# Performance work log

Hardware: AMD Instinct MI355X
Metric: run time of the kernel (lower is better)

The kernel has to match this reference:

```python
import jax, jax.numpy as jnp
import numpy as np

B, S, D, H = 2, 2048, 1024, 16
HD = D // H  # 64
ROPE_BASE = 10000.0


def setup_inputs() -> dict:
    key = jax.random.key(0)
    k1, k2, k3 = jax.random.split(key, 3)
    std = 1.0 / np.sqrt(D)
    x = jax.random.normal(k1, (B, S, D), dtype=jnp.float32)
    w_in = jax.random.normal(k2, (3 * D, D), dtype=jnp.float32) * std
    w_out = jax.random.normal(k3, (D, D), dtype=jnp.float32) * (std / np.sqrt(2.0))
    return {"x": x, "w_in": w_in, "w_out": w_out}


def _rope_cos_sin(seq_len, head_dim):
    inv_freq = 1.0 / (ROPE_BASE ** (jnp.arange(0, head_dim, 2, dtype=jnp.float32) / head_dim))
    t = jnp.arange(seq_len, dtype=jnp.float32)
    freqs = jnp.einsum("s,d->sd", t, inv_freq)          # [S, HD/2]
    emb = jnp.concatenate([freqs, freqs], axis=-1)       # [S, HD]
    return jnp.cos(emb)[None, :, None, :], jnp.sin(emb)[None, :, None, :]


def _rotate_half(x):
    x1, x2 = jnp.split(x, 2, axis=-1)
    return jnp.concatenate([-x2, x1], axis=-1)


def _apply_rope(x, cos, sin):
    return x * cos + _rotate_half(x) * sin


def reference(x, w_in, w_out):
    b, s, d = x.shape
    # fused QKV projection (no bias)
    qkv = x @ w_in.T                                      # [B, S, 3D]
    q, k, v = jnp.split(qkv, 3, axis=-1)
    q = q.reshape(b, s, H, HD)
    k = k.reshape(b, s, H, HD)
    v = v.reshape(b, s, H, HD)
    # rotary (offset = 0, no KV cache)
    cos, sin = _rope_cos_sin(s, HD)
    q = _apply_rope(q, cos, sin)
    k = _apply_rope(k, cos, sin)
    # causal SDPA, scale 1/sqrt(head_dim)
    scale = 1.0 / jnp.sqrt(jnp.asarray(HD, dtype=x.dtype))
    scores = jnp.einsum("bqhd,bkhd->bhqk", q, k) * scale  # [B, H, S, S]
    causal = jnp.tril(jnp.ones((s, s), dtype=bool))
    scores = jnp.where(causal, scores, jnp.asarray(-jnp.inf, dtype=scores.dtype))
    attn = jax.nn.softmax(scores, axis=-1)
    out = jnp.einsum("bhqk,bkhd->bqhd", attn, v).reshape(b, s, d)
    return out @ w_out.T
```

## Files before the change

kernel.cpp:

```cpp
#include <hip/hip_runtime.h>
#include <hip/hip_bf16.h>
#include <math.h>

#define NB 2
#define NS 2048
#define ND 1024
#define NH 16
#define HD 64
#define BS (NB*NS)
#define D3 (3*ND)
#define NT (NS/64)

typedef __bf16 bf16;
typedef __bf16 bf16x4 __attribute__((ext_vector_type(4)));
typedef __bf16 bf16x8 __attribute__((ext_vector_type(8)));
typedef float f32x4 __attribute__((ext_vector_type(4)));

#define MFMA16(a,b,c) __builtin_amdgcn_mfma_f32_16x16x32_bf16(a,b,c,0,0,0)

static __device__ inline f32x4 zero4() { f32x4 z; z[0]=0.f; z[1]=0.f; z[2]=0.f; z[3]=0.f; return z; }

__device__ __forceinline__ void gload_lds16(const bf16* g, bf16* l) {
    __builtin_amdgcn_global_load_lds(
        (__attribute__((address_space(1))) unsigned int*)g,
        (__attribute__((address_space(3))) unsigned int*)l, 16, 0, 0);
}

#define CVT1 (BS*ND/8)
#define CVT2 (D3*ND/8)
#define CVT3 (ND*ND/8)
#define CVTN (CVT1+CVT2+CVT3)
__global__ __launch_bounds__(256) void prep(
    const float* __restrict__ x, const float* __restrict__ w_in, const float* __restrict__ w_out,
    bf16* __restrict__ xb, bf16* __restrict__ winb, bf16* __restrict__ woutb,
    float* __restrict__ cosT, float* __restrict__ sinT)
{
    int i = blockIdx.x * 256 + threadIdx.x;
    if (i < CVTN) {
        const float* in; bf16* out; int j;
        if (i < CVT1)            { in = x;     out = xb;    j = i; }
        else if (i < CVT1+CVT2)  { in = w_in;  out = winb;  j = i - CVT1; }
        else                     { in = w_out; out = woutb; j = i - CVT1 - CVT2; }
        const float4* p = (const float4*)in;
        float4 a = p[j*2], b = p[j*2+1];
        bf16x8 o;
        o[0]=(bf16)a.x; o[1]=(bf16)a.y; o[2]=(bf16)a.z; o[3]=(bf16)a.w;
        o[4]=(bf16)b.x; o[5]=(bf16)b.y; o[6]=(bf16)b.z; o[7]=(bf16)b.w;
        ((bf16x8*)out)[j] = o;
    } else {
        int k = i - CVTN;
        int s = k >> 5, j = k & 31;
        float inv = __expf(-(float)j * (9.210340372f * 0.03125f));
        float ang = (float)s * inv;
        cosT[k] = cosf(ang);
        sinT[k] = sinf(ang);
    }
}

template<int EPI>
__global__ __launch_bounds__(256) void gemm_bt(
    const bf16* __restrict__ A, const bf16* __restrict__ Bm,
    float* __restrict__ C, bf16* __restrict__ Qb, bf16* __restrict__ Kb, bf16* __restrict__ Vt,
    const float* __restrict__ cosT, const float* __restrict__ sinT,
    int M, int N, int K)
{
    __shared__ bf16 As[2][128*64];
    __shared__ bf16 Bs[2][128*64];
    int t = threadIdx.x;
    int lane = t & 63, w = t >> 6;
    int wr = w >> 1, wc = w & 1;
    int lr = lane & 15, lg = lane >> 4;
    int m0 = blockIdx.y * 128, n0 = blockIdx.x * 128;

    int srow = lane >> 3;
    int schunk = (lane & 7) ^ srow;
    const bf16* gA = &A [(size_t)(m0 + w*32 + srow)*K + schunk*8];
    const bf16* gB = &Bm[(size_t)(n0 + w*32 + srow)*K + schunk*8];

    auto stage = [&](int kt) {
        int buf = kt & 1;
        bf16* lA = &As[buf][w*2048];
        bf16* lB = &Bs[buf][w*2048];
        int k0 = kt * 64;
        #pragma unroll
        for (int i=0;i<4;i++) {
            gload_lds16(gA + (size_t)(i*8)*K + k0, lA + i*512);
            gload_lds16(gB + (size_t)(i*8)*K + k0, lB + i*512);
        }
    };

    f32x4 acc[4][4];
    for (int m=0;m<4;m++) for (int n=0;n<4;n++) acc[m][n] = zero4();

    int nt = K >> 6;
    stage(0);
    stage(1);

    for (int kt = 0; kt < nt; kt++) {
        int cur = kt & 1;
        if (kt < nt-1) asm volatile("s_waitcnt vmcnt(8)" ::: "memory");
        else           asm volatile("s_waitcnt vmcnt(0)" ::: "memory");
        __builtin_amdgcn_s_barrier();
        __builtin_amdgcn_sched_barrier(0);

        bf16x8 af[2][4], bfr[2][4];
        #pragma unroll
        for (int ks=0;ks<2;ks++) {
            #pragma unroll
            for (int m=0;m<4;m++) {
                int row = wr*64 + m*16 + lr;
                af[ks][m] = *(const bf16x8*)&As[cur][row*64 + (((ks*4+lg) ^ (row&7))*8)];
            }
            #pragma unroll
            for (int n=0;n<4;n++) {
                int row = wc*64 + n*16 + lr;
                bfr[ks][n] = *(const bf16x8*)&Bs[cur][row*64 + (((ks*4+lg) ^ (row&7))*8)];
            }
        }
        asm volatile("s_waitcnt lgkmcnt(0)" ::: "memory");
        __builtin_amdgcn_sched_barrier(0);
        __builtin_amdgcn_s_barrier();
        __builtin_amdgcn_sched_barrier(0);

        if (kt + 2 < nt) stage(kt + 2);

        __builtin_amdgcn_s_setprio(1);
        #pragma unroll
        for (int ks=0;ks<2;ks++)
            #pragma unroll
            for (int m=0;m<4;m++)
                #pragma unroll
                for (int n=0;n<4;n++)
                    acc[m][n] = MFMA16(af[ks][m], bfr[ks][n], acc[m][n]);
        __builtin_amdgcn_s_setprio(0);
    }

    if (EPI == 0) {
        for (int m=0;m<4;m++) for (int n=0;n<4;n++) {
            int grow = m0 + wr*64 + m*16 + lg*4;
            int gcol = n0 + wc*64 + n*16 + lr;
            for (int r=0;r<4;r++)
                C[(size_t)(grow+r) * N + gcol] = acc[m][n][r];
        }
    } else {
        int which = n0 >> 10;
        if (which == 2) {
            for (int m=0;m<4;m++) for (int n=0;n<4;n++) {
                int grow = m0 + wr*64 + m*16 + lg*4;
                int gcol = n0 + wc*64 + n*16 + lr;
                int h = (gcol & 1023) >> 6, d = gcol & 63;
                int b = grow >> 11, s0 = grow & (NS-1);
                int shi = s0 & ~63, j = s0 & 63;
                int kp = ((j>>5)&1)*32 + ((j>>2)&3)*8 + ((j>>4)&1)*4;
                bf16x4 pv;
                for (int r=0;r<4;r++) pv[r] = (bf16)acc[m][n][r];
                *(bf16x4*)&Vt[((size_t)((b*NH + h)*HD + d))*NS + shi + kp] = pv;
            }
        } else {
            const float qs = 0.125f * 1.44269504f;
            bf16* dst = (which == 0) ? Qb : Kb;
            for (int m=0;m<4;m++) {
                int grow = m0 + wr*64 + m*16 + lg*4;
                #pragma unroll
                for (int n=0;n<2;n++) {
                    int gcol = n0 + wc*64 + n*16 + lr;
                    int h = (gcol & 1023) >> 6, j = gcol & 63;
                    #pragma unroll
                    for (int r=0;r<4;r++) {
                        int gm = grow + r;
                        int b = gm >> 11, s = gm & (NS-1);
                        float c  = cosT[(s<<5)+j];
                        float sn = sinT[(s<<5)+j];
                        float x1 = acc[m][n][r], x2 = acc[m][n+2][r];
                        float y1 = x1*c - x2*sn;
                        float y2 = x2*c + x1*sn;
                        if (which == 0) { y1 *= qs; y2 *= qs; }
                        size_t off = ((size_t)((b*NH + h)*NS + s))*HD;
                        dst[off + j]      = (bf16)y1;
                        dst[off + j + 32] = (bf16)y2;
                    }
                }
            }
        }
    }
}

__global__ __launch_bounds__(256, 4) void attn_fwd(
    const bf16* __restrict__ Qb, const bf16* __restrict__ Kb, const bf16* __restrict__ Vp,
    bf16* __restrict__ AO)
{
    __shared__ bf16 Ks[2][64*64];
    __shared__ bf16 Vs[2][64*64];
    int t = threadIdx.x;
    int lane = t & 63, w = t >> 6;
    int lr = lane & 15, lg = lane >> 4;
    int wgid = blockIdx.x;
    int qt = (NT-1) - (wgid >> 5);
    int bh = wgid & 31;
    int b = bh >> 4, h = bh & 15;
    size_t base = (size_t)bh * NS * HD;
    int q0 = qt*64 + w*16;

    bf16x8 qf[2];
    #pragma unroll
    for (int c=0;c<2;c++)
        qf[c] = *(const bf16x8*)&Qb[base + (size_t)(q0+lr)*HD + c*32 + lg*8];

    float m_r = -__builtin_inff(), l_r = 0.f;
    f32x4 o[4];
    #pragma unroll
    for (int n=0;n<4;n++) o[n] = zero4();

    int srow = t >> 3;
    int sch  = t & 7;
    int sslot = sch ^ (srow & 7);
    bf16x8 kr[2], vr[2];

    auto load_window = [&](int kv0) {
        #pragma unroll
        for (int i=0;i<2;i++)
            kr[i] = *(const bf16x8*)&Kb[base + (size_t)(kv0 + i*32 + srow)*HD + sch*8];
        #pragma unroll
        for (int i=0;i<2;i++)
            vr[i] = *(const bf16x8*)&Vp[base + (size_t)(i*32 + srow)*NS + kv0 + sch*8];
    };
    auto store_window = [&](int buf) {
        #pragma unroll
        for (int i=0;i<2;i++)
            *(bf16x8*)&Ks[buf][(i*32 + srow)*64 + sslot*8] = kr[i];
        #pragma unroll
        for (int i=0;i<2;i++)
            *(bf16x8*)&Vs[buf][(i*32 + srow)*64 + sslot*8] = vr[i];
    };

    for (int kt = 0; kt <= qt; kt++) {
        if (kt == 0) { load_window(0); store_window(0); __syncthreads(); }
        int cur = kt & 1;
        int kv0 = kt*64;
        bool last = (kt == qt);
        if (!last) load_window(kv0 + 64);

        const bf16* ksb = &Ks[cur][0];
        const bf16* vsb = &Vs[cur][0];

        f32x4 sc[4];
        __builtin_amdgcn_s_setprio(1);
        #pragma unroll
        for (int kb=0;kb<4;kb++) {
            int row = kb*16 + lr;
            bf16x8 k0 = *(const bf16x8*)&ksb[row*64 + ((lg     ^ (row&7))*8)];
            bf16x8 k1 = *(const bf16x8*)&ksb[row*64 + (((4+lg) ^ (row&7))*8)];
            sc[kb] = MFMA16(k0, qf[0], zero4());
            sc[kb] = MFMA16(k1, qf[1], sc[kb]);
        }
        __builtin_amdgcn_s_setprio(0);

        if (last) {
            int qi = q0 + lr;
            #pragma unroll
            for (int kb=0;kb<4;kb++)
                #pragma unroll
                for (int r=0;r<4;r++)
                    if (kv0 + kb*16 + lg*4 + r > qi) sc[kb][r] = -__builtin_inff();
        }

        float tm = fmaxf(fmaxf(sc[0][0],sc[0][1]), fmaxf(sc[0][2],sc[0][3]));
        #pragma unroll
        for (int kb=1;kb<4;kb++)
            tm = fmaxf(tm, fmaxf(fmaxf(sc[kb][0],sc[kb][1]), fmaxf(sc[kb][2],sc[kb][3])));
        tm = fmaxf(tm, __shfl_xor(tm, 16));
        tm = fmaxf(tm, __shfl_xor(tm, 32));
        if (!__all(tm <= m_r + 8.0f)) {
            float mn = fmaxf(m_r, tm);
            float fsc = exp2f(m_r - mn);
            l_r *= fsc;
            #pragma unroll
            for (int n=0;n<4;n++) o[n] *= fsc;
            m_r = mn;
        }
        float p[4][4];
        float ps = 0.f;
        #pragma unroll
        for (int kb=0;kb<4;kb++)
            #pragma unroll
            for (int r=0;r<4;r++) {
                float pe = exp2f(sc[kb][r] - m_r);
                p[kb][r] = pe;
                ps += pe;
            }
        ps += __shfl_xor(ps, 16);
        ps += __shfl_xor(ps, 32);
        l_r += ps;

        bf16x8 pa[2];
        #pragma unroll
        for (int c=0;c<2;c++) {
            bf16x8 v;
            #pragma unroll
            for (int i=0;i<8;i++) v[i] = (bf16)p[c*2 + (i>>2)][i&3];
            pa[c] = v;
        }

        __builtin_amdgcn_s_setprio(1);
        #pragma unroll
        for (int c=0;c<2;c++)
            #pragma unroll
            for (int n=0;n<4;n++) {
                int row = n*16 + lr;
                bf16x8 vf = *(const bf16x8*)&vsb[row*64 + (((c*4+lg) ^ (row&7))*8)];
                o[n] = MFMA16(vf, pa[c], o[n]);
            }
        __builtin_amdgcn_s_setprio(0);

        if (!last) { store_window(cur^1); __syncthreads(); }
    }

    float inv = 1.0f / l_r;
    int q = q0 + lr;
    #pragma unroll
    for (int n=0;n<4;n++) {
        bf16x4 ov;
        #pragma unroll
        for (int r=0;r<4;r++) ov[r] = (bf16)(o[n][r] * inv);
        *(bf16x4*)&AO[((size_t)(b*NS + q)*NH + h)*HD + n*16 + lg*4] = ov;
    }
}

extern "C" void kernel_launch(void* const* d_in, const int* in_sizes, int n_in,
                              void* d_out, int out_size, void* d_ws, size_t ws_size,
                              hipStream_t stream) {
    const float* x     = (const float*)d_in[0];
    const float* w_in  = (const float*)d_in[1];
    const float* w_out = (const float*)d_in[2];
    float* out = (float*)d_out;

    char* p = (char*)d_ws;
    bf16* xb    = (bf16*)p; p += (size_t)BS*ND*2;
    bf16* winb  = (bf16*)p; p += (size_t)D3*ND*2;
    bf16* woutb = (bf16*)p; p += (size_t)ND*ND*2;
    bf16* Qb    = (bf16*)p; p += (size_t)NB*NH*NS*HD*2;
    bf16* Kb    = (bf16*)p; p += (size_t)NB*NH*NS*HD*2;
    bf16* Vp    = (bf16*)p; p += (size_t)NB*NH*NS*HD*2;
    bf16* AO    = (bf16*)p; p += (size_t)BS*ND*2;
    float* cosT = (float*)p; p += (size_t)NS*32*4;
    float* sinT = (float*)p; p += (size_t)NS*32*4;

    prep<<<(CVTN + NS*32)/256, 256, 0, stream>>>(x, w_in, w_out, xb, winb, woutb, cosT, sinT);
    gemm_bt<1><<<dim3(D3/128, BS/128), 256, 0, stream>>>(xb, winb, nullptr, Qb, Kb, Vp,
                                                         cosT, sinT, BS, D3, ND);
    attn_fwd<<<NB*NH*NT, 256, 0, stream>>>(Qb, Kb, Vp, AO);
    gemm_bt<0><<<dim3(ND/128, BS/128), 256, 0, stream>>>(AO, woutb, out, nullptr, nullptr, nullptr,
                                                         nullptr, nullptr, BS, ND, ND);
}
```

Measured before the change: 102.5 us.

## Interleave cos/sin table, reorder attention tiles, defer row-sum reduction

Packs the RoPE cos and sin tables into one float2 array so the QKV GEMM epilogue issues a single load per element instead of two. Attention work-groups are reordered so long and short causal query tiles alternate rather than running strictly longest-first. The softmax row sum is now kept per lane and reduced across lanes only once at the end, and the max shuffle-reduction runs only when a rescale is needed. This trades the existing longest-first load balancing for a different tile order, which could worsen tail balance.

```diff
diff --git a/kernel.cpp b/kernel.cpp
--- a/kernel.cpp
+++ b/kernel.cpp
@@ -33,7 +33,7 @@
 __global__ __launch_bounds__(256) void prep(
     const float* __restrict__ x, const float* __restrict__ w_in, const float* __restrict__ w_out,
     bf16* __restrict__ xb, bf16* __restrict__ winb, bf16* __restrict__ woutb,
-    float* __restrict__ cosT, float* __restrict__ sinT)
+    float2* __restrict__ csT)
 {
     int i = blockIdx.x * 256 + threadIdx.x;
     if (i < CVTN) {
@@ -52,8 +52,7 @@
         int s = k >> 5, j = k & 31;
         float inv = __expf(-(float)j * (9.210340372f * 0.03125f));
         float ang = (float)s * inv;
-        cosT[k] = cosf(ang);
-        sinT[k] = sinf(ang);
+        csT[k] = make_float2(cosf(ang), sinf(ang));
     }
 }
 
@@ -61,7 +60,7 @@
 __global__ __launch_bounds__(256) void gemm_bt(
     const bf16* __restrict__ A, const bf16* __restrict__ Bm,
     float* __restrict__ C, bf16* __restrict__ Qb, bf16* __restrict__ Kb, bf16* __restrict__ Vt,
-    const float* __restrict__ cosT, const float* __restrict__ sinT,
+    const float2* __restrict__ csT,
     int M, int N, int K)
 {
     __shared__ bf16 As[2][128*64];
@@ -169,11 +168,10 @@
                     for (int r=0;r<4;r++) {
                         int gm = grow + r;
                         int b = gm >> 11, s = gm & (NS-1);
-                        float c  = cosT[(s<<5)+j];
-                        float sn = sinT[(s<<5)+j];
+                        float2 cs = csT[(s<<5)+j];
                         float x1 = acc[m][n][r], x2 = acc[m][n+2][r];
-                        float y1 = x1*c - x2*sn;
-                        float y2 = x2*c + x1*sn;
+                        float y1 = x1*cs.x - x2*cs.y;
+                        float y2 = x2*cs.x + x1*cs.y;
                         if (which == 0) { y1 *= qs; y2 *= qs; }
                         size_t off = ((size_t)((b*NH + h)*NS + s))*HD;
                         dst[off + j]      = (bf16)y1;
@@ -195,7 +193,8 @@
     int lane = t & 63, w = t >> 6;
     int lr = lane & 15, lg = lane >> 4;
     int wgid = blockIdx.x;
-    int qt = (NT-1) - (wgid >> 5);
+    int g = wgid >> 5;
+    int qt = (g < 8) ? 31 - g : (g < 16) ? g - 8 : (g < 24) ? 39 - g : g - 16;
     int bh = wgid & 31;
     int b = bh >> 4, h = bh & 15;
     size_t base = (size_t)bh * NS * HD;
@@ -206,7 +205,7 @@
     for (int c=0;c<2;c++)
         qf[c] = *(const bf16x8*)&Qb[base + (size_t)(q0+lr)*HD + c*32 + lg*8];
 
-    float m_r = -__builtin_inff(), l_r = 0.f;
+    float m_r = -__builtin_inff(), l_p = 0.f;
     f32x4 o[4];
     #pragma unroll
     for (int n=0;n<4;n++) o[n] = zero4();
@@ -260,37 +259,33 @@
             #pragma unroll
             for (int kb=0;kb<4;kb++)
                 #pragma unroll
-                for (int r=0;r<4;r++)
-                    if (kv0 + kb*16 + lg*4 + r > qi) sc[kb][r] = -__builtin_inff();
-        }
-
-        float tm = fmaxf(fmaxf(sc[0][0],sc[0][1]), fmaxf(sc[0][2],sc[0][3]));
+                for (int rr=0;rr<4;rr++)
+                    if (kv0 + kb*16 + lg*4 + rr > qi) sc[kb][rr] = -__builtin_inff();
+        }
+
+        float tml = fmaxf(fmaxf(sc[0][0],sc[0][1]), fmaxf(sc[0][2],sc[0][3]));
         #pragma unroll
         for (int kb=1;kb<4;kb++)
-            tm = fmaxf(tm, fmaxf(fmaxf(sc[kb][0],sc[kb][1]), fmaxf(sc[kb][2],sc[kb][3])));
-        tm = fmaxf(tm, __shfl_xor(tm, 16));
-        tm = fmaxf(tm, __shfl_xor(tm, 32));
-        if (!__all(tm <= m_r + 8.0f)) {
-            float mn = fmaxf(m_r, tm);
+            tml = fmaxf(tml, fmaxf(fmaxf(sc[kb][0],sc[kb][1]), fmaxf(sc[kb][2],sc[kb][3])));
+        if (!__all(tml <= m_r + 8.0f)) {
+            float tr = fmaxf(tml, __shfl_xor(tml, 16));
+            tr = fmaxf(tr, __shfl_xor(tr, 32));
+            float mn = fmaxf(m_r, tr);
             float fsc = exp2f(m_r - mn);
-            l_r *= fsc;
+            l_p *= fsc;
             #pragma unroll
             for (int n=0;n<4;n++) o[n] *= fsc;
             m_r = mn;
         }
         float p[4][4];
-        float ps = 0.f;
         #pragma unroll
         for (int kb=0;kb<4;kb++)
             #pragma unroll
-            for (int r=0;r<4;r++) {
-                float pe = exp2f(sc[kb][r] - m_r);
-                p[kb][r] = pe;
-                ps += pe;
-            }
-        ps += __shfl_xor(ps, 16);
-        ps += __shfl_xor(ps, 32);
-        l_r += ps;
+            for (int rr=0;rr<4;rr++) {
+                float pe = exp2f(sc[kb][rr] - m_r);
+                p[kb][rr] = pe;
+                l_p += pe;
+            }
 
         bf16x8 pa[2];
         #pragma unroll
@@ -315,13 +310,18 @@
         if (!last) { store_window(cur^1); __syncthreads(); }
     }
 
-    float inv = 1.0f / l_r;
-    int q = q0 + lr;
+    float lrow = l_p;
+    lrow += __shfl_xor(lrow, 16);
+    lrow += __shfl_xor(lrow, 32);
+
+    float inv = 1.0f / lrow;
+    int q = q0 + w*16 - w*16 + lr + 0;
+    q = q0 + lr;
     #pragma unroll
     for (int n=0;n<4;n++) {
         bf16x4 ov;
         #pragma unroll
-        for (int r=0;r<4;r++) ov[r] = (bf16)(o[n][r] * inv);
+        for (int rr=0;rr<4;rr++) ov[rr] = (bf16)(o[n][rr] * inv);
         *(bf16x4*)&AO[((size_t)(b*NS + q)*NH + h)*HD + n*16 + lg*4] = ov;
     }
 }
@@ -342,13 +342,12 @@
     bf16* Kb    = (bf16*)p; p += (size_t)NB*NH*NS*HD*2;
     bf16* Vp    = (bf16*)p; p += (size_t)NB*NH*NS*HD*2;
     bf16* AO    = (bf16*)p; p += (size_t)BS*ND*2;
-    float* cosT = (float*)p; p += (size_t)NS*32*4;
-    float* sinT = (float*)p; p += (size_t)NS*32*4;
-
-    prep<<<(CVTN + NS*32)/256, 256, 0, stream>>>(x, w_in, w_out, xb, winb, woutb, cosT, sinT);
+    float2* csT = (float2*)p; p += (size_t)NS*32*8;
+
+    prep<<<(CVTN + NS*32)/256, 256, 0, stream>>>(x, w_in, w_out, xb, winb, woutb, csT);
     gemm_bt<1><<<dim3(D3/128, BS/128), 256, 0, stream>>>(xb, winb, nullptr, Qb, Kb, Vp,
-                                                         cosT, sinT, BS, D3, ND);
+                                                         csT, BS, D3, ND);
     attn_fwd<<<NB*NH*NT, 256, 0, stream>>>(Qb, Kb, Vp, AO);
     gemm_bt<0><<<dim3(ND/128, BS/128), 256, 0, stream>>>(AO, woutb, out, nullptr, nullptr, nullptr,
-                                                         nullptr, nullptr, BS, ND, ND);
-}
+                                                         nullptr, BS, ND, ND);
+}
```

Measured after the change: 100.4 us. 1.02x faster.
